# Optimization experiments

Hardware: AMD Instinct MI355X
Metric: run time of the kernel (lower is better)

Reference implementation:

```python
import jax, jax.numpy as jnp
import numpy as np

B, N, D = 256, 50, 128
NEG = -9e15  # torch uses -9000000000000000.0
LEAKY_SLOPE = 0.2


def setup_inputs() -> dict:
    key = jax.random.key(0)
    ks = jax.random.split(key, 6)
    hidden = jax.random.normal(ks[0], (B, N, D), dtype=jnp.float32)
    adj = jax.random.randint(ks[1], (B, N, N), 0, 5)  # edge types 0..4
    a_0 = jax.random.normal(ks[2], (D, 1), dtype=jnp.float32) * 0.05
    a_1 = jax.random.normal(ks[3], (D, 1), dtype=jnp.float32) * 0.05
    a_2 = jax.random.normal(ks[4], (D, 1), dtype=jnp.float32) * 0.05
    a_3 = jax.random.normal(ks[5], (D, 1), dtype=jnp.float32) * 0.05
    return {"hidden": hidden, "adj": adj, "a_0": a_0, "a_1": a_1, "a_2": a_2, "a_3": a_3}


def reference(hidden, adj, a_0, a_1, a_2, a_3):
    # LocalAggregator.forward (typed-edge GAT over session graph).
    # Original builds a_input[b,i,j,:] = h[b,i,:]*h[b,j,:] (B,N,N,D) then
    # projects with 4 relation vectors a_k (D,1). We fuse: stack the 4
    # vectors and contract D in one einsum -> e[b,k,i,j].
    A = jnp.concatenate([a_0, a_1, a_2, a_3], axis=1)          # (D, 4)
    e = jnp.einsum('bid,bjd,dk->bkij', hidden, hidden, A)      # (B, 4, N, N)
    e = jax.nn.leaky_relu(e, negative_slope=LEAKY_SLOPE)
    # Per-edge-type masking: adj value v in {1..4} selects branch v-1,
    # anything else gets -9e15 (same chained torch.where semantics/order).
    scores = jnp.full_like(e[:, 0], NEG)                        # (B, N, N)
    scores = jnp.where(adj == 1, e[:, 0], scores)
    scores = jnp.where(adj == 2, e[:, 1], scores)
    scores = jnp.where(adj == 3, e[:, 2], scores)
    scores = jnp.where(adj == 4, e[:, 3], scores)
    attn = jax.nn.softmax(scores, axis=-1)                      # (B, N, N)
    return jnp.einsum('bij,bjd->bid', attn, hidden)             # (B, N, D)
```

## Files before the change

### kernel.cpp

```cpp
#include <hip/hip_runtime.h>
#include <stdint.h>

typedef __attribute__((ext_vector_type(8))) short short8;
typedef __attribute__((ext_vector_type(4))) float f32x4;

namespace {
constexpr int   kN     = 50;
constexpr int   kD     = 128;
constexpr float kNeg   = -9.0e15f;
constexpr float kSlope = 0.2f;
constexpr int   HS32   = 132;
constexpr int   HS16   = 136;
constexpr int   ADS    = 52;
constexpr int   PS     = 20;
}

union Pack8 { uint32_t u[4]; short8 s; };

__global__ __launch_bounds__(256)
void gat_v10_kernel(const float* __restrict__ hidden,
                    const int*   __restrict__ adj,
                    const float* __restrict__ a0,
                    const float* __restrict__ a1,
                    const float* __restrict__ a2,
                    const float* __restrict__ a3,
                    float* __restrict__ out)
{
    __shared__ float          Hf [kN * HS32];
    __shared__ unsigned short Hhi[64 * HS16];
    __shared__ unsigned short Hlo[64 * HS16];
    __shared__ unsigned char  Ad [kN * ADS];
    __shared__ unsigned short Pw [4][64 * PS];

    const int b    = blockIdx.x;
    const int tid  = threadIdx.x;
    const int lane = tid & 63;
    const int wid  = __builtin_amdgcn_readfirstlane(tid >> 6);
    const int g    = lane >> 4;
    const int f    = lane & 15;

    const float* __restrict__ hb   = hidden + (size_t)b * (kN * kD);
    const int*   __restrict__ adjb = adj    + (size_t)b * (kN * kN);
    float*       __restrict__ outb = out    + (size_t)b * (kN * kD);

    const float4* hg = reinterpret_cast<const float4*>(hb);
    #pragma unroll
    for (int it8 = 0; it8 < 8; ++it8) {
        const int idx = tid + it8 * 256;
        const int j   = idx >> 5;
        const int d4  = idx & 31;
        float4 v = make_float4(0.f, 0.f, 0.f, 0.f);
        if (j < kN) v = hg[j * 32 + d4];

        const uint32_t h0 = __float_as_uint(v.x) & 0xffff0000u;
        const uint32_t h1 = __float_as_uint(v.y) & 0xffff0000u;
        const uint32_t h2 = __float_as_uint(v.z) & 0xffff0000u;
        const uint32_t h3 = __float_as_uint(v.w) & 0xffff0000u;
        uint2 hiw;
        hiw.x = h1 | (h0 >> 16);
        hiw.y = h3 | (h2 >> 16);
        const float r0 = v.x - __uint_as_float(h0);
        const float r1 = v.y - __uint_as_float(h1);
        const float r2 = v.z - __uint_as_float(h2);
        const float r3 = v.w - __uint_as_float(h3);
        uint2 low;
        low.x = (__float_as_uint(r1) & 0xffff0000u) | (__float_as_uint(r0) >> 16);
        low.y = (__float_as_uint(r3) & 0xffff0000u) | (__float_as_uint(r2) >> 16);
        *reinterpret_cast<uint2*>(&Hhi[j * HS16 + 4 * d4]) = hiw;
        *reinterpret_cast<uint2*>(&Hlo[j * HS16 + 4 * d4]) = low;
        if (j < kN) *reinterpret_cast<float4*>(&Hf[j * HS32 + 4 * d4]) = v;
    }
    for (int idx = tid; idx < 625; idx += 256) {
        const int4 v = reinterpret_cast<const int4*>(adjb)[idx];
        const int e = 4 * idx;
        const int vv[4] = {v.x, v.y, v.z, v.w};
        #pragma unroll
        for (int p = 0; p < 4; ++p) {
            const int ee  = e + p;
            const int row = ee / kN;
            const int col = ee - kN * row;
            Ad[row * ADS + col] = (unsigned char)vv[p];
        }
    }
    __syncthreads();

    const int i0   = 16 * wid;
    const int irow = (i0 + f < kN) ? (i0 + f) : (kN - 1);

    f32x4 acc[4][4];
    #pragma unroll
    for (int jt = 0; jt < 4; ++jt)
        #pragma unroll
        for (int k = 0; k < 4; ++k) acc[jt][k] = (f32x4){0.f, 0.f, 0.f, 0.f};

    const float* __restrict__ aks[4] = {a0, a1, a2, a3};

    #pragma unroll
    for (int ksl = 0; ksl < 4; ++ksl) {
        const int dofs = 32 * ksl + 8 * g;

        const float4 hA0 = *reinterpret_cast<const float4*>(&Hf[irow * HS32 + dofs]);
        const float4 hA1 = *reinterpret_cast<const float4*>(&Hf[irow * HS32 + dofs + 4]);
        const float ha[8] = {hA0.x, hA0.y, hA0.z, hA0.w, hA1.x, hA1.y, hA1.z, hA1.w};

        short8 qh[4], ql[4];
        #pragma unroll
        for (int k = 0; k < 4; ++k) {
            const float4 av0 = *reinterpret_cast<const float4*>(aks[k] + dofs);
            const float4 av1 = *reinterpret_cast<const float4*>(aks[k] + dofs + 4);
            const float aa[8] = {av0.x, av0.y, av0.z, av0.w, av1.x, av1.y, av1.z, av1.w};
            Pack8 ph, pl;
            #pragma unroll
            for (int p = 0; p < 4; ++p) {
                const float q0 = ha[2 * p]     * aa[2 * p];
                const float q1 = ha[2 * p + 1] * aa[2 * p + 1];
                const uint32_t b0 = __float_as_uint(q0) & 0xffff0000u;
                const uint32_t b1 = __float_as_uint(q1) & 0xffff0000u;
                ph.u[p] = b1 | (b0 >> 16);
                const float s0 = q0 - __uint_as_float(b0);
                const float s1 = q1 - __uint_as_float(b1);
                pl.u[p] = (__float_as_uint(s1) & 0xffff0000u) | (__float_as_uint(s0) >> 16);
            }
            qh[k] = ph.s;
            ql[k] = pl.s;
        }

        #pragma unroll
        for (int jt = 0; jt < 4; ++jt) {
            const int jrow = 16 * jt + f;
            const short8 bh = *reinterpret_cast<const short8*>(&Hhi[jrow * HS16 + dofs]);
            const short8 bl = *reinterpret_cast<const short8*>(&Hlo[jrow * HS16 + dofs]);
            #pragma unroll
            for (int k = 0; k < 4; ++k) {
                acc[jt][k] = __builtin_amdgcn_mfma_f32_16x16x32_bf16(qh[k], bh, acc[jt][k], 0, 0, 0);
                acc[jt][k] = __builtin_amdgcn_mfma_f32_16x16x32_bf16(qh[k], bl, acc[jt][k], 0, 0, 0);
                acc[jt][k] = __builtin_amdgcn_mfma_f32_16x16x32_bf16(ql[k], bh, acc[jt][k], 0, 0, 0);
            }
        }
    }

    float s[4][4];
    #pragma unroll
    for (int jt = 0; jt < 4; ++jt) {
        const int j = 16 * jt + f;
        #pragma unroll
        for (int reg = 0; reg < 4; ++reg) {
            const int ii  = i0 + 4 * g + reg;
            const int iic = (ii < kN) ? ii : (kN - 1);
            int kv = 0;
            if (j < kN) kv = Ad[iic * ADS + j];
            const float x = (kv == 1) ? acc[jt][0][reg]
                          : (kv == 2) ? acc[jt][1][reg]
                          : (kv == 3) ? acc[jt][2][reg]
                          : (kv == 4) ? acc[jt][3][reg] : 0.f;
            const float lx = (x > 0.f) ? x : kSlope * x;
            s[jt][reg] = (kv >= 1 && kv <= 4) ? lx : kNeg;
        }
    }

    #pragma unroll
    for (int reg = 0; reg < 4; ++reg) {
        float m = fmaxf(fmaxf(s[0][reg], s[1][reg]), fmaxf(s[2][reg], s[3][reg]));
        #pragma unroll
        for (int o = 1; o < 16; o <<= 1) m = fmaxf(m, __shfl_xor(m, o));

        float e[4];
        float t = 0.f;
        #pragma unroll
        for (int jt = 0; jt < 4; ++jt) {
            const int j = 16 * jt + f;
            e[jt] = (j < kN) ? __expf(s[jt][reg] - m) : 0.f;
            t += e[jt];
        }
        #pragma unroll
        for (int o = 1; o < 16; o <<= 1) t += __shfl_xor(t, o);

        const float inv = 1.0f / t;
        #pragma unroll
        for (int jt = 0; jt < 4; ++jt) {
            uint32_t u = __float_as_uint(e[jt] * inv);
            u += 0x7fffu + ((u >> 16) & 1u);
            Pw[wid][(16 * jt + f) * PS + 4 * g + reg] = (unsigned short)(u >> 16);
        }
    }

    #pragma unroll
    for (int dh = 0; dh < 2; ++dh) {
        const int db = 64 * dh + 4 * f;
        f32x4 o0 = {0.f, 0.f, 0.f, 0.f}, o1 = o0, o2 = o0, o3 = o0;
        #pragma unroll 5
        for (int j = 0; j < kN; ++j) {
            const float4  hv = *reinterpret_cast<const float4*>(&Hf[j * HS32 + db]);
            const ushort4 p4 = *reinterpret_cast<const ushort4*>(&Pw[wid][j * PS + 4 * g]);
            const float av0 = __uint_as_float(((uint32_t)p4.x) << 16);
            const float av1 = __uint_as_float(((uint32_t)p4.y) << 16);
            const float av2 = __uint_as_float(((uint32_t)p4.z) << 16);
            const float av3 = __uint_as_float(((uint32_t)p4.w) << 16);
            o0.x += av0 * hv.x; o0.y += av0 * hv.y; o0.z += av0 * hv.z; o0.w += av0 * hv.w;
            o1.x += av1 * hv.x; o1.y += av1 * hv.y; o1.z += av1 * hv.z; o1.w += av1 * hv.w;
            o2.x += av2 * hv.x; o2.y += av2 * hv.y; o2.z += av2 * hv.z; o2.w += av2 * hv.w;
            o3.x += av3 * hv.x; o3.y += av3 * hv.y; o3.z += av3 * hv.z; o3.w += av3 * hv.w;
        }
        const int rbase = i0 + 4 * g;
        if (rbase + 0 < kN) *reinterpret_cast<f32x4*>(&outb[(rbase + 0) * kD + db]) = o0;
        if (rbase + 1 < kN) *reinterpret_cast<f32x4*>(&outb[(rbase + 1) * kD + db]) = o1;
        if (rbase + 2 < kN) *reinterpret_cast<f32x4*>(&outb[(rbase + 2) * kD + db]) = o2;
        if (rbase + 3 < kN) *reinterpret_cast<f32x4*>(&outb[(rbase + 3) * kD + db]) = o3;
    }
}

extern "C" void kernel_launch(void* const* d_in, const int* in_sizes, int n_in,
                              void* d_out, int out_size, void* d_ws, size_t ws_size,
                              hipStream_t stream) {
    const float* hidden = reinterpret_cast<const float*>(d_in[0]);
    const int*   adjp   = reinterpret_cast<const int*>(d_in[1]);
    const float* a0     = reinterpret_cast<const float*>(d_in[2]);
    const float* a1     = reinterpret_cast<const float*>(d_in[3]);
    const float* a2     = reinterpret_cast<const float*>(d_in[4]);
    const float* a3     = reinterpret_cast<const float*>(d_in[5]);
    float*       outp   = reinterpret_cast<float*>(d_out);

    gat_v10_kernel<<<dim3(256), dim3(256), 0, stream>>>(
        hidden, adjp, a0, a1, a2, a3, outp);
}
```

Before: 18.33 us.

## Split D reduction across two wave groups with LDS partial-score exchange

Doubles the block to 512 threads (8 waves). Each pair of waves shares a 16-row tile and splits the 128-wide D contraction into halves, then exchanges partial scores through a new LDS buffer behind an extra barrier. Each wave computes the full softmax redundantly but produces only its half of the output columns. This shortens each wave's serial MFMA chain and output loop, but costs more LDS and adds a block-wide sync and redundant softmax work.

```diff
diff --git a/kernel.cpp b/kernel.cpp
--- a/kernel.cpp
+++ b/kernel.cpp
@@ -17,8 +17,8 @@
 
 union Pack8 { uint32_t u[4]; short8 s; };
 
-__global__ __launch_bounds__(256)
-void gat_v10_kernel(const float* __restrict__ hidden,
+__global__ __launch_bounds__(512)
+void gat_v11_kernel(const float* __restrict__ hidden,
                     const int*   __restrict__ adj,
                     const float* __restrict__ a0,
                     const float* __restrict__ a1,
@@ -30,7 +30,8 @@
     __shared__ unsigned short Hhi[64 * HS16];
     __shared__ unsigned short Hlo[64 * HS16];
     __shared__ unsigned char  Ad [kN * ADS];
-    __shared__ unsigned short Pw [4][64 * PS];
+    __shared__ float          Xch[8][64][16];
+    __shared__ unsigned short Pw [8][64 * PS];
 
     const int b    = blockIdx.x;
     const int tid  = threadIdx.x;
@@ -45,8 +46,8 @@
 
     const float4* hg = reinterpret_cast<const float4*>(hb);
     #pragma unroll
-    for (int it8 = 0; it8 < 8; ++it8) {
-        const int idx = tid + it8 * 256;
+    for (int it4 = 0; it4 < 4; ++it4) {
+        const int idx = tid + it4 * 512;
         const int j   = idx >> 5;
         const int d4  = idx & 31;
         float4 v = make_float4(0.f, 0.f, 0.f, 0.f);
@@ -70,7 +71,7 @@
         *reinterpret_cast<uint2*>(&Hlo[j * HS16 + 4 * d4]) = low;
         if (j < kN) *reinterpret_cast<float4*>(&Hf[j * HS32 + 4 * d4]) = v;
     }
-    for (int idx = tid; idx < 625; idx += 256) {
+    for (int idx = tid; idx < 625; idx += 512) {
         const int4 v = reinterpret_cast<const int4*>(adjb)[idx];
         const int e = 4 * idx;
         const int vv[4] = {v.x, v.y, v.z, v.w};
@@ -84,7 +85,9 @@
     }
     __syncthreads();
 
-    const int i0   = 16 * wid;
+    const int it   = wid & 3;
+    const int kh   = wid >> 2;
+    const int i0   = 16 * it;
     const int irow = (i0 + f < kN) ? (i0 + f) : (kN - 1);
 
     f32x4 acc[4][4];
@@ -96,8 +99,8 @@
     const float* __restrict__ aks[4] = {a0, a1, a2, a3};
 
     #pragma unroll
-    for (int ksl = 0; ksl < 4; ++ksl) {
-        const int dofs = 32 * ksl + 8 * g;
+    for (int ksl2 = 0; ksl2 < 2; ++ksl2) {
+        const int dofs = 64 * kh + 32 * ksl2 + 8 * g;
 
         const float4 hA0 = *reinterpret_cast<const float4*>(&Hf[irow * HS32 + dofs]);
         const float4 hA1 = *reinterpret_cast<const float4*>(&Hf[irow * HS32 + dofs + 4]);
@@ -139,7 +142,8 @@
         }
     }
 
-    float s[4][4];
+    f32x4 spart[4];
+    uint32_t vmask = 0;
     #pragma unroll
     for (int jt = 0; jt < 4; ++jt) {
         const int j = 16 * jt + f;
@@ -149,12 +153,29 @@
             const int iic = (ii < kN) ? ii : (kN - 1);
             int kv = 0;
             if (j < kN) kv = Ad[iic * ADS + j];
-            const float x = (kv == 1) ? acc[jt][0][reg]
-                          : (kv == 2) ? acc[jt][1][reg]
-                          : (kv == 3) ? acc[jt][2][reg]
-                          : (kv == 4) ? acc[jt][3][reg] : 0.f;
+            const bool valid = (kv >= 1) && (kv <= 4);
+            spart[jt][reg] = (kv == 1) ? acc[jt][0][reg]
+                           : (kv == 2) ? acc[jt][1][reg]
+                           : (kv == 3) ? acc[jt][2][reg]
+                           : (kv == 4) ? acc[jt][3][reg] : 0.f;
+            vmask |= (valid ? 1u : 0u) << (4 * jt + reg);
+        }
+    }
+
+    #pragma unroll
+    for (int jt = 0; jt < 4; ++jt)
+        *reinterpret_cast<f32x4*>(&Xch[wid][lane][4 * jt]) = spart[jt];
+    __syncthreads();
+
+    float s[4][4];
+    #pragma unroll
+    for (int jt = 0; jt < 4; ++jt) {
+        const f32x4 o = *reinterpret_cast<const f32x4*>(&Xch[wid ^ 4][lane][4 * jt]);
+        #pragma unroll
+        for (int reg = 0; reg < 4; ++reg) {
+            const float x  = spart[jt][reg] + o[reg];
             const float lx = (x > 0.f) ? x : kSlope * x;
-            s[jt][reg] = (kv >= 1 && kv <= 4) ? lx : kNeg;
+            s[jt][reg] = ((vmask >> (4 * jt + reg)) & 1u) ? lx : kNeg;
         }
     }
 
@@ -184,9 +205,8 @@
         }
     }
 
-    #pragma unroll
-    for (int dh = 0; dh < 2; ++dh) {
-        const int db = 64 * dh + 4 * f;
+    {
+        const int db = 64 * kh + 4 * f;
         f32x4 o0 = {0.f, 0.f, 0.f, 0.f}, o1 = o0, o2 = o0, o3 = o0;
         #pragma unroll 5
         for (int j = 0; j < kN; ++j) {
@@ -220,6 +240,6 @@
     const float* a3     = reinterpret_cast<const float*>(d_in[5]);
     float*       outp   = reinterpret_cast<float*>(d_out);
 
-    gat_v10_kernel<<<dim3(256), dim3(256), 0, stream>>>(
+    gat_v11_kernel<<<dim3(256), dim3(512), 0, stream>>>(
         hidden, adjp, a0, a1, a2, a3, outp);
 }
```

Result: faster. 17.76 us (-3.1%).
